# Performance work log

Hardware: AMD Instinct MI355X
Metric: run time of the kernel (lower is better)

Reference implementation:

```python
import jax, jax.numpy as jnp
import numpy as np

B, S, HID = 2, 2048, 2048
H, HKV, D = 16, 8, 128
CHUNK = 512
THETA = 1000000.0
NEG = -1e9


def setup_inputs() -> dict:
    key = jax.random.key(0)
    ks = jax.random.split(key, 10)
    hidden_states = jax.random.normal(ks[0], (B, S, HID), dtype=jnp.float32)
    # additive causal mask (0 on/below diagonal, -1e9 above)
    tri = jnp.tril(jnp.ones((S, S), dtype=bool))
    attention_mask = jnp.where(tri, 0.0, NEG).astype(jnp.float32)
    attention_mask = jnp.broadcast_to(attention_mask[None, None], (B, 1, S, S))
    w = 0.02
    Wq = jax.random.normal(ks[1], (HID, H * D), dtype=jnp.float32) * w
    bq = jax.random.normal(ks[2], (H * D,), dtype=jnp.float32) * w
    Wk = jax.random.normal(ks[3], (HID, HKV * D), dtype=jnp.float32) * w
    bk = jax.random.normal(ks[4], (HKV * D,), dtype=jnp.float32) * w
    Wv = jax.random.normal(ks[5], (HID, HKV * D), dtype=jnp.float32) * w
    bv = jax.random.normal(ks[6], (HKV * D,), dtype=jnp.float32) * w
    Wo = jax.random.normal(ks[7], (H * D, HID), dtype=jnp.float32) * w
    bo = jax.random.normal(ks[8], (HID,), dtype=jnp.float32) * w
    return {"hidden_states": hidden_states, "attention_mask": attention_mask,
            "Wq": Wq, "bq": bq, "Wk": Wk, "bk": bk, "Wv": Wv, "bv": bv,
            "Wo": Wo, "bo": bo}


def _rope_tables(seq_len, dim):
    inv_freq = 1.0 / (THETA ** (jnp.arange(0, dim, 2, dtype=jnp.float32) / dim))
    pos = jnp.arange(seq_len, dtype=jnp.float32)
    freqs = pos[:, None] * inv_freq[None, :]          # [S, D/2]
    emb = jnp.concatenate([freqs, freqs], axis=-1)    # [S, D]
    return jnp.cos(emb)[None, None], jnp.sin(emb)[None, None]  # [1,1,S,D]


def _rotate_half(x):
    x1, x2 = jnp.split(x, 2, axis=-1)
    return jnp.concatenate([-x2, x1], axis=-1)


def _attn_forward(hidden_states, attention_mask, Wq, bq, Wk, bk, Wv, bv, Wo, bo):
    bsz, s, _ = hidden_states.shape
    q = (hidden_states @ Wq + bq).reshape(bsz, s, H, D).transpose(0, 2, 1, 3)
    k = (hidden_states @ Wk + bk).reshape(bsz, s, HKV, D).transpose(0, 2, 1, 3)
    v = (hidden_states @ Wv + bv).reshape(bsz, s, HKV, D).transpose(0, 2, 1, 3)
    cos, sin = _rope_tables(s, D)
    q = q * cos + _rotate_half(q) * sin
    k = k * cos + _rotate_half(k) * sin
    n_rep = H // HKV
    k = jnp.repeat(k, n_rep, axis=1)  # repeat_kv
    v = jnp.repeat(v, n_rep, axis=1)
    scale = 1.0 / jnp.sqrt(jnp.float32(D))
    nq, nk = s // CHUNK, s // CHUNK
    Qc = q.reshape(bsz, H, nq, CHUNK, D)
    Kc = jnp.moveaxis(k.reshape(bsz, H, nk, CHUNK, D), 2, 0)   # [nk,B,H,Ck,D]
    Vc = jnp.moveaxis(v.reshape(bsz, H, nk, CHUNK, D), 2, 0)
    Mc = jnp.moveaxis(attention_mask.reshape(bsz, 1, nq, CHUNK, nk, CHUNK), 4, 0)  # [nk,B,1,nq,Cq,Ck]

    def step(carry, xs):
        o, m, d = carry
        k_seg, v_seg, m_seg = xs
        # scores: [B,H,nq,Cq,Ck]
        sc = jnp.einsum('bhqcd,bhkd->bhqck', Qc, k_seg) * scale + m_seg
        new_m = jnp.maximum(m, sc.max(axis=-1, keepdims=True))
        e = jnp.exp(sc - new_m)
        sums = e.sum(axis=-1, keepdims=True)
        prev = jnp.exp(m - new_m)          # NOTE: uses running max, as in source
        d_new = prev + sums
        o = (o * prev + jnp.einsum('bhqck,bhkd->bhqcd', e, v_seg)) / d_new
        return (o, new_m, d_new), None

    o0 = jnp.zeros((bsz, H, nq, CHUNK, D), dtype=jnp.float32)
    m0 = jnp.full((bsz, H, nq, CHUNK, 1), -jnp.inf, dtype=jnp.float32)
    d0 = jnp.ones((bsz, H, nq, CHUNK, 1), dtype=jnp.float32)
    (o, m, d), _ = jax.lax.scan(step, (o0, m0, d0), (Kc, Vc, Mc))
    # final rescale: attn_output * exp(max - logsumexp) == o / d_last (source math)
    o = o / d
    attn = o.reshape(bsz, H, s, D).transpose(0, 2, 1, 3).reshape(bsz, s, H * D)
    return attn @ Wo + bo


def reference(hidden_states, attention_mask, Wq, bq, Wk, bk, Wv, bv, Wo, bo):
    return _attn_forward(hidden_states, attention_mask, Wq, bq, Wk, bk, Wv, bv, Wo, bo)
```

## Files before the change

kernel.cpp:

```cpp
#include <hip/hip_runtime.h>
#include <hip/hip_bf16.h>


typedef __attribute__((ext_vector_type(8))) short s8v;
typedef __attribute__((ext_vector_type(4))) float f4v;
typedef __attribute__((ext_vector_type(4))) unsigned int u32x4;

#define MFMA16(a, b, c) __builtin_amdgcn_mfma_f32_16x16x32_bf16((a), (b), (c), 0, 0, 0)

typedef unsigned short u16;
typedef const __attribute__((address_space(1))) unsigned int* gas_p;
typedef __attribute__((address_space(3))) unsigned int* las_p;

template <bool B> struct BoolC { static constexpr bool value = B; };

__device__ __forceinline__ void gl_lds16(const void* g, void* l) {
    __builtin_amdgcn_global_load_lds((gas_p)g, (las_p)l, 16, 0, 0);
}

__device__ __forceinline__ u16 f2b(float f) {
    __hip_bfloat16 h = __float2bfloat16(f);
    return *reinterpret_cast<u16*>(&h);
}
__device__ __forceinline__ float b2f(u16 u) {
    __hip_bfloat16 h;
    *reinterpret_cast<u16*>(&h) = u;
    return __bfloat162float(h);
}

__device__ __forceinline__ void qswap(unsigned int& a, unsigned int& b) {
#if __has_builtin(__builtin_amdgcn_permlane32_swap) && __has_builtin(__builtin_amdgcn_permlane16_swap)
    typedef __attribute__((ext_vector_type(2))) unsigned int u32x2;
    u32x2 r1 = __builtin_amdgcn_permlane32_swap(a, b, false, false);
    u32x2 r2 = __builtin_amdgcn_permlane16_swap(r1[0], r1[1], false, false);
    a = r2[0]; b = r2[1];
#else
    asm volatile("v_permlane32_swap_b32 %0, %1\n\t"
                 "s_nop 0\n\t"
                 "v_permlane16_swap_b32 %0, %1\n\t"
                 "s_nop 0"
                 : "+v"(a), "+v"(b));
#endif
}

__device__ const unsigned char qt_tab[40] = {
    4, 5, 6, 7,
    8, 8, 9, 9, 10, 10, 11, 11,
    12, 12, 12, 13, 13, 13, 14, 14, 14, 15, 15, 15,
    3, 7, 11, 15, 2, 6, 10, 14, 1, 5, 9, 13, 0, 4, 8, 12};
__device__ const unsigned char c_tab[40] = {
    0, 0, 0, 0,
    0, 1, 0, 1, 0, 1, 0, 1,
    0, 1, 2, 0, 1, 2, 0, 1, 2, 0, 1, 2,
    0, 1, 2, 3, 0, 1, 2, 3, 0, 1, 2, 3, 0, 1, 2, 3};

__device__ __forceinline__ int uoff40(int qt, int c) {
    int qc = qt >> 2;
    if (c < qc) {
        if (qt < 8) return qt - 4;
        if (qt < 12) return 4 + ((qt - 8) << 1) + c;
        return 12 + (qt - 12) * 3 + c;
    }
    return 24 + ((3 - (qt & 3)) << 2) + qc;
}

__global__ __launch_bounds__(256) void k_cast_hs(const float* __restrict__ src,
                                                 u16* __restrict__ dst) {
    int i = blockIdx.x * 256 + threadIdx.x;
    float4 v = reinterpret_cast<const float4*>(src)[i];
    alignas(8) u16 t[4] = {f2b(v.x), f2b(v.y), f2b(v.z), f2b(v.w)};
    reinterpret_cast<uint2*>(dst)[i] = *reinterpret_cast<uint2*>(t);
}

__global__ __launch_bounds__(256) void k_transpose_w(
    const float* __restrict__ Wq, const float* __restrict__ Wk,
    const float* __restrict__ Wv, const float* __restrict__ Wo,
    u16* __restrict__ wt_all, u16* __restrict__ wo_t) {
    int id = blockIdx.x;
    const float* W; u16* dst; int N, nbase;
    if (id < 4096)      { W = Wq; dst = wt_all; N = 2048; nbase = 0; }
    else if (id < 6144) { W = Wk; dst = wt_all; N = 1024; nbase = 2048; id -= 4096; }
    else if (id < 8192) { W = Wv; dst = wt_all; N = 1024; nbase = 3072; id -= 6144; }
    else                { W = Wo; dst = wo_t;  N = 2048; nbase = 0;    id -= 8192; }
    int tiles_n = N >> 5;
    int k0 = (id / tiles_n) << 5, n0 = (id % tiles_n) << 5;
    __shared__ float t[32][33];
    int tid = threadIdx.x;
    {
        int row = tid >> 3, c4 = (tid & 7) << 2;
        float4 v = *reinterpret_cast<const float4*>(&W[(size_t)(k0 + row) * N + n0 + c4]);
        t[row][c4 + 0] = v.x; t[row][c4 + 1] = v.y;
        t[row][c4 + 2] = v.z; t[row][c4 + 3] = v.w;
    }
    __syncthreads();
    {
        int n = tid >> 3, kq = (tid & 7) << 2;
        alignas(8) u16 p[4];
#pragma unroll
        for (int j = 0; j < 4; j++) p[j] = f2b(t[kq + j][n]);
        *reinterpret_cast<uint2*>(&dst[(size_t)(nbase + n0 + n) * 2048 + k0 + kq]) =
            *reinterpret_cast<uint2*>(p);
    }
}

__global__ __launch_bounds__(256) void k_bias(const float* __restrict__ bq,
                                              const float* __restrict__ bk,
                                              const float* __restrict__ bv,
                                              float* __restrict__ dst) {
    int i = blockIdx.x * 256 + threadIdx.x;
    float v = (i < 2048) ? bq[i] : (i < 3072) ? bk[i - 2048] : bv[i - 3072];
    dst[i] = v;
}

__global__ __launch_bounds__(256) void k_gemm(
    const u16* __restrict__ A, const u16* __restrict__ Bt,
    const float* __restrict__ bias, void* __restrict__ out,
    int M, int N, int K, int out_f32) {
    __shared__ alignas(16) u16 As[2][128][64];
    __shared__ alignas(16) u16 Bs[2][128][64];
    int tid = threadIdx.x;
    int wave = tid >> 6, lane = tid & 63, quad = lane >> 4, l16 = lane & 15;
    int nwg = gridDim.x * gridDim.y;
    int wg = blockIdx.y * gridDim.x + blockIdx.x;
    int l = (wg & 7) * (nwg >> 3) + (wg >> 3);
    int t4 = l >> 4, a4 = l & 15;
    int tn4 = gridDim.x >> 2;
    int tm = t4 / tn4, tn = t4 % tn4;
    int m0 = ((tm << 2) + (a4 >> 2)) << 7;
    int n0 = ((tn << 2) + (a4 & 3)) << 7;
    int wm = (wave >> 1) << 6, wn = (wave & 1) << 6;
    f4v zero = {0.f, 0.f, 0.f, 0.f};
    f4v acc[4][4];
#pragma unroll
    for (int a = 0; a < 4; a++)
#pragma unroll
        for (int b = 0; b < 4; b++) acc[a][b] = zero;
    int r0 = tid >> 3;
    int gsw = (tid & 7) ^ (r0 & 7);
    const u16* gA = A + (size_t)(m0 + r0) * K + (gsw << 3);
    const u16* gB = Bt + (size_t)(n0 + r0) * K + (gsw << 3);
    auto stage = [&](int k0, int buf) {
#pragma unroll
        for (int i = 0; i < 4; i++) {
            gl_lds16(gA + (size_t)(i << 5) * K + k0,
                     (char*)&As[buf][0][0] + (i << 12) + tid * 16);
            gl_lds16(gB + (size_t)(i << 5) * K + k0,
                     (char*)&Bs[buf][0][0] + (i << 12) + tid * 16);
        }
    };
    int NT = K >> 6;
    stage(0, 0);
    __syncthreads();
    for (int t = 0; t < NT; t++) {
        int cur = t & 1;
        if (t + 1 < NT) stage((t + 1) << 6, cur ^ 1);
#pragma unroll
        for (int ks = 0; ks < 2; ks++) {
            int rg = (((ks << 2) | quad) ^ (l16 & 7)) << 3;
            s8v af[4], bf_[4];
#pragma unroll
            for (int mi = 0; mi < 4; mi++)
                af[mi] = *reinterpret_cast<const s8v*>(&As[cur][wm + mi * 16 + l16][rg]);
#pragma unroll
            for (int ni = 0; ni < 4; ni++)
                bf_[ni] = *reinterpret_cast<const s8v*>(&Bs[cur][wn + ni * 16 + l16][rg]);
#pragma unroll
            for (int mi = 0; mi < 4; mi++)
#pragma unroll
                for (int ni = 0; ni < 4; ni++)
                    acc[mi][ni] = MFMA16(af[mi], bf_[ni], acc[mi][ni]);
        }
        __syncthreads();
    }
    if (!out_f32) {
        u16* cs = &As[0][0][0];
#pragma unroll
        for (int ni = 0; ni < 4; ni++) {
            float bsv = bias[n0 + wn + ni * 16 + l16];
#pragma unroll
            for (int mi = 0; mi < 4; mi++)
#pragma unroll
                for (int r = 0; r < 4; r++)
                    cs[(wm + mi * 16 + (quad << 2) + r) * 128 + wn + ni * 16 + l16] =
                        f2b(acc[mi][ni][r] + bsv);
        }
        __syncthreads();
        int row = tid >> 1, c0 = (tid & 1) << 6;
        u16* dst = (u16*)out + (size_t)(m0 + row) * N + n0 + c0;
#pragma unroll
        for (int j = 0; j < 8; j++)
            *reinterpret_cast<uint4*>(dst + j * 8) =
                *reinterpret_cast<const uint4*>(&cs[row * 128 + c0 + j * 8]);
    } else {
        float* cf = (float*)&As[0][0][0];
#pragma unroll
        for (int p = 0; p < 2; p++) {
            __syncthreads();
            if ((wm >> 6) == p) {
#pragma unroll
                for (int ni = 0; ni < 4; ni++) {
                    float bsv = bias[n0 + wn + ni * 16 + l16];
#pragma unroll
                    for (int mi = 0; mi < 4; mi++)
#pragma unroll
                        for (int r = 0; r < 4; r++)
                            cf[((wm - (p << 6)) + mi * 16 + (quad << 2) + r) * 128 +
                               wn + ni * 16 + l16] = acc[mi][ni][r] + bsv;
                }
            }
            __syncthreads();
            int row = tid >> 2, q4 = (tid & 3) << 5;
            float* dst = (float*)out + (size_t)(m0 + (p << 6) + row) * N + n0 + q4;
#pragma unroll
            for (int j = 0; j < 8; j++)
                *reinterpret_cast<uint4*>(dst + j * 4) =
                    *reinterpret_cast<const uint4*>(&cf[row * 128 + q4 + j * 4]);
        }
    }
}

__global__ __launch_bounds__(256) void k_rope(const u16* __restrict__ qkv,
                                              u16* __restrict__ qr,
                                              u16* __restrict__ kr) {
    const float qscale = 0.08838834764831845f * 1.44269504088896340f;
    int row = blockIdx.x;
    int b = row >> 11, s = row & 2047;
    const u16* src = qkv + (size_t)row * 4096;
    __shared__ float lcs[64], lsn[64];
    int tid = threadIdx.x;
    if (tid < 64) {
        float fr = (float)s * exp2f((float)tid * -0.31143075889569023f);
        lcs[tid] = cosf(fr);
        lsn[tid] = sinf(fr);
    }
    __syncthreads();
    for (int u = tid; u < 1536; u += 256) {
        int hh, i;
        const u16* sp;
        u16* dp;
        float sc;
        if (u < 1024) {
            hh = u >> 6; i = u & 63;
            sp = src + hh * 128;
            dp = qr + ((size_t)(b * 16 + hh) * 2048 + s) * 128;
            sc = qscale;
        } else {
            int u2 = u - 1024;
            hh = u2 >> 6; i = u2 & 63;
            sp = src + 2048 + hh * 128;
            dp = kr + ((size_t)(b * 8 + hh) * 2048 + s) * 128;
            sc = 1.f;
        }
        float x1 = b2f(sp[i]);
        float x2 = b2f(sp[i + 64]);
        float cs = lcs[i], sn = lsn[i];
        dp[i]      = f2b((x1 * cs - x2 * sn) * sc);
        dp[i + 64] = f2b((x2 * cs + x1 * sn) * sc);
    }
}

__global__ __launch_bounds__(256) void k_vtrans(const u16* __restrict__ qkv,
                                                u16* __restrict__ vt) {
    int bkv = blockIdx.z, b = bkv >> 3, kv = bkv & 7;
    int s0 = blockIdx.x << 6, d0 = blockIdx.y << 5;
    __shared__ alignas(16) u16 t[32][72];
    int tid = threadIdx.x, c = tid & 31, rr = tid >> 5;
#pragma unroll
    for (int i = 0; i < 8; i++) {
        int s = s0 + rr + i * 8;
        t[c][rr + i * 8] = qkv[(size_t)(b * 2048 + s) * 4096 + 3072 + kv * 128 + d0 + c];
    }
    __syncthreads();
    int dd = tid >> 3, sc8 = (tid & 7) << 3;
    *reinterpret_cast<uint4*>(&vt[((size_t)(b * 8 + kv) * 128 + d0 + dd) * 2048 + s0 + sc8]) =
        *reinterpret_cast<const uint4*>(&t[dd][sc8]);
}

__global__ __launch_bounds__(256, 3) void k_attn_part(const u16* __restrict__ qr,
                                                      const u16* __restrict__ kr,
                                                      const u16* __restrict__ vt,
                                                      u16* __restrict__ PVp,
                                                      float* __restrict__ scp) {
    const float NINF = -__builtin_inff();
    __shared__ alignas(16) u16 Ks[2][64 * 128];
    __shared__ alignas(16) u16 Vs[128 * 64];

    int tid = threadIdx.x;
    int wv = tid >> 6, lane = tid & 63, quad = lane >> 4, l16 = lane & 15;
    int x = blockIdx.x, h = blockIdx.y, b = blockIdx.z, kvh = h >> 1;
    int qt = qt_tab[x], c = c_tab[x], qc = qt >> 2;
    bool diag = (c == qc);
    int m3 = qt & 3;
    int nt = diag ? ((m3 + 1) << 1) : 8;
    int kbase = c << 9;
    const u16* Qp = qr + ((size_t)(b * 16 + h) * 2048 + qt * 128 + wv * 32) * 128;
    const u16* Kp = kr + ((size_t)(b * 8 + kvh) * 2048) * 128;
    const u16* Vp = vt + ((size_t)(b * 8 + kvh) * 128) * 2048;

    s8v qf0[4], qf1[4];
#pragma unroll
    for (int sl = 0; sl < 4; sl++) {
        qf0[sl] = *reinterpret_cast<const s8v*>(&Qp[l16 * 128 + sl * 32 + (quad << 3)]);
        qf1[sl] = *reinterpret_cast<const s8v*>(&Qp[(16 + l16) * 128 + sl * 32 + (quad << 3)]);
    }
    s8v ones;
#pragma unroll
    for (int i = 0; i < 8; i++) ones[i] = (short)0x3F80;
    s8v pzero;
#pragma unroll
    for (int i = 0; i < 8; i++) pzero[i] = (short)0;

    int krow = tid >> 4, kg = (tid & 15) ^ krow;
    int vd = tid >> 3, vg = (tid & 7) ^ (vd & 7);
    auto stageK = [&](int t) {
        int kbt = kbase + (t << 6);
        const u16* kgp = Kp + (size_t)(kbt + krow) * 128 + (kg << 3);
        char* kd = (char*)&Ks[t & 1][0];
#pragma unroll
        for (int i = 0; i < 4; i++)
            gl_lds16(kgp + (size_t)(i << 4) * 128, kd + (i << 12) + tid * 16);
    };
    auto stageV = [&](int t) {
        int kbt = kbase + (t << 6);
        const u16* vgp = Vp + (size_t)vd * 2048 + kbt + (vg << 3);
        char* vdst = (char*)&Vs[0];
#pragma unroll
        for (int i = 0; i < 4; i++)
            gl_lds16(vgp + (size_t)(i << 5) * 2048, vdst + (i << 12) + tid * 16);
    };

    auto pack = [&](const f4v& s, bool tri, bool act, float& tmx,
                    unsigned int& wlo, unsigned int& whi) {
        if (!act) { wlo = 0u; whi = 0u; return; }
        float e[4];
#pragma unroll
        for (int r = 0; r < 4; r++) {
            float v = s[r];
            if (tri && ((quad << 2) + r > l16)) v = NINF;
            tmx = fmaxf(tmx, v);
            e[r] = __builtin_amdgcn_exp2f(v);
        }
        wlo = (unsigned int)f2b(e[0]) | ((unsigned int)f2b(e[1]) << 16);
        whi = (unsigned int)f2b(e[2]) | ((unsigned int)f2b(e[3]) << 16);
    };

    f4v zero = {0.f, 0.f, 0.f, 0.f};
    f4v u0[8], u1[8], sums0 = zero, sums1 = zero;
#pragma unroll
    for (int ni = 0; ni < 8; ni++) { u0[ni] = zero; u1[ni] = zero; }
    float tmx0 = NINF, tmx1 = NINF;
    int qg0 = wv << 1, qg1 = (wv << 1) + 1;

    auto run = [&](auto diagc) {
        constexpr bool DIAG = decltype(diagc)::value;
        stageK(0);
        for (int t = 0; t < nt; t++) {
            __syncthreads();
            stageV(t);
            if (t + 1 < nt) stageK(t + 1);
            const char* Kbuf = (const char*)&Ks[t & 1][0];
            int kgb = DIAG ? ((t << 2) - (m3 << 3)) : 0;
            s8v pa0s[2], pa1s[2];
            bool act0[2], act1[2];
#pragma unroll
            for (int s2 = 0; s2 < 2; s2++) {
                int kgA = kgb + (s2 << 1), kgB = kgA + 1;
                bool skip = DIAG && (kgA > qg1);
                bool a0 = !DIAG || (kgA <= qg0);
                bool b0 = !DIAG || (kgB <= qg0);
                bool b1 = !DIAG || (kgB <= qg1);
                act1[s2] = !skip;
                act0[s2] = !skip && a0;
                if (skip) { pa0s[s2] = pzero; pa1s[s2] = pzero; continue; }
                f4v sA0 = zero, sA1 = zero, sB0 = zero, sB1 = zero;
#pragma unroll
                for (int sl = 0; sl < 4; sl++) {
                    s8v kf = *reinterpret_cast<const s8v*>(
                        Kbuf + (((s2 << 1) << 4) + l16) * 256 +
                        ((((sl << 2) + quad) ^ l16) << 4));
                    if (a0) sA0 = MFMA16(kf, qf0[sl], sA0);
                    sA1 = MFMA16(kf, qf1[sl], sA1);
                }
                if (b1) {
#pragma unroll
                    for (int sl = 0; sl < 4; sl++) {
                        s8v kf = *reinterpret_cast<const s8v*>(
                            Kbuf + ((((s2 << 1) | 1) << 4) + l16) * 256 +
                            ((((sl << 2) + quad) ^ l16) << 4));
                        if (b0) sB0 = MFMA16(kf, qf0[sl], sB0);
                        sB1 = MFMA16(kf, qf1[sl], sB1);
                    }
                }
                unsigned int A0w, A1w, B0w, B1w;
                pack(sA1, DIAG && (kgA == qg1), true, tmx1, A0w, A1w);
                pack(sB1, DIAG && (kgB == qg1), b1, tmx1, B0w, B1w);
                qswap(A0w, B0w); qswap(A1w, B1w);
                u32x4 pw1 = {A0w, A1w, B0w, B1w};
                pa1s[s2] = __builtin_bit_cast(s8v, pw1);
                if (a0) {
                    unsigned int C0w, C1w, D0w, D1w;
                    pack(sA0, DIAG && (kgA == qg0), true, tmx0, C0w, C1w);
                    pack(sB0, DIAG && (kgB == qg0), b0, tmx0, D0w, D1w);
                    qswap(C0w, D0w); qswap(C1w, D1w);
                    u32x4 pw0 = {C0w, C1w, D0w, D1w};
                    pa0s[s2] = __builtin_bit_cast(s8v, pw0);
                } else {
                    pa0s[s2] = pa1s[s2];
                }
            }
            __syncthreads();
#pragma unroll
            for (int s2 = 0; s2 < 2; s2++) {
                if (DIAG && !act1[s2]) continue;
                bool a0 = !DIAG || act0[s2];
                if (a0) sums0 = MFMA16(pa0s[s2], ones, sums0);
                sums1 = MFMA16(pa1s[s2], ones, sums1);
#pragma unroll
                for (int ni = 0; ni < 8; ni++) {
                    s8v vf = *reinterpret_cast<const s8v*>(
                        (const char*)&Vs[0] + ((ni << 4) + l16) * 128 +
                        ((((s2 << 2) + quad) ^ (l16 & 7)) << 4));
                    if (a0) u0[ni] = MFMA16(pa0s[s2], vf, u0[ni]);
                    u1[ni] = MFMA16(pa1s[s2], vf, u1[ni]);
                }
            }
        }
    };
    if (diag) run(BoolC<true>{}); else run(BoolC<false>{});

    tmx0 = fmaxf(tmx0, __shfl_xor(tmx0, 16));
    tmx0 = fmaxf(tmx0, __shfl_xor(tmx0, 32));
    tmx1 = fmaxf(tmx1, __shfl_xor(tmx1, 16));
    tmx1 = fmaxf(tmx1, __shfl_xor(tmx1, 32));
    float m0[4], m1[4], resc0[4], resc1[4];
#pragma unroll
    for (int r = 0; r < 4; r++) {
        m0[r] = __shfl(tmx0, (quad << 2) + r);
        m1[r] = __shfl(tmx1, (quad << 2) + r);
        resc0[r] = __builtin_amdgcn_exp2f(-m0[r]);
        resc1[r] = __builtin_amdgcn_exp2f(-m1[r]);
    }
    int slot = (b * 16 + h) * 40 + x;
    u16* pvdst = PVp + (size_t)slot * 16384;
    int row0 = wv * 32 + (quad << 2);
#pragma unroll
    for (int ni = 0; ni < 8; ni++)
#pragma unroll
        for (int r = 0; r < 4; r++) {
            pvdst[(row0 + r) * 128 + ni * 16 + l16] = f2b(u0[ni][r] * resc0[r]);
            pvdst[(row0 + 16 + r) * 128 + ni * 16 + l16] = f2b(u1[ni][r] * resc1[r]);
        }
    if (l16 == 0) {
        float* scd = scp + (size_t)slot * 256 + row0;
#pragma unroll
        for (int r = 0; r < 4; r++) {
            scd[r] = m0[r] * 0.6931471805599453f;
            scd[16 + r] = m1[r] * 0.6931471805599453f;
            scd[128 + r] = sums0[r] * resc0[r];
            scd[144 + r] = sums1[r] * resc1[r];
        }
    }
}

__global__ __launch_bounds__(256) void k_attn_comb(const u16* __restrict__ PVp,
                                                   const float* __restrict__ scp,
                                                   u16* __restrict__ attnb) {
    int qt64 = blockIdx.x, h = blockIdx.y, b = blockIdx.z;
    int qt = qt64 >> 1, qc = qt >> 2;
    int tid = threadIdx.x;
    int row = ((qt64 & 1) << 6) + (tid >> 2), d0 = (tid & 3) << 5;
    int bh = b * 16 + h;
    float o[32];
#pragma unroll
    for (int i = 0; i < 32; i++) o[i] = 0.f;
    float mprev = -__builtin_inff(), dlast = 1.f;
    for (int cc = 0; cc <= qc; cc++) {
        int slot = bh * 40 + uoff40(qt, cc);
        float ch = scp[(size_t)slot * 256 + row];
        float sh = scp[(size_t)slot * 256 + 128 + row];
        float mnew = fmaxf(mprev, ch);
        float p = __expf(mprev - mnew);
        float lam = __expf(ch - mnew);
        float dd = p + lam * sh;
        float inv = 1.f / dd;
        const u16* pv = PVp + (size_t)slot * 16384 + row * 128 + d0;
#pragma unroll
        for (int k = 0; k < 4; k++) {
            s8v v8 = *reinterpret_cast<const s8v*>(pv + (k << 3));
#pragma unroll
            for (int j = 0; j < 8; j++) {
                int i = (k << 3) + j;
                o[i] = (o[i] * p + lam * b2f((u16)v8[j])) * inv;
            }
        }
        mprev = mnew;
        dlast = dd;
    }
    if (qc == 3) {
        float inv = 1.f / dlast;
#pragma unroll
        for (int i = 0; i < 32; i++) o[i] *= inv;
    }
    alignas(16) u16 ob[32];
#pragma unroll
    for (int i = 0; i < 32; i++) ob[i] = f2b(o[i]);
    u16* dst = attnb + (size_t)(b * 2048 + qt * 128 + row) * 2048 + h * 128 + d0;
#pragma unroll
    for (int k = 0; k < 4; k++)
        reinterpret_cast<uint4*>(dst)[k] = reinterpret_cast<const uint4*>(ob)[k];
}

extern "C" void kernel_launch(void* const* d_in, const int* in_sizes, int n_in,
                              void* d_out, int out_size, void* d_ws, size_t ws_size,
                              hipStream_t stream) {
    (void)in_sizes; (void)n_in; (void)out_size; (void)ws_size;
    const float* hs = (const float*)d_in[0];
    const float* Wq = (const float*)d_in[2];
    const float* bq = (const float*)d_in[3];
    const float* Wk = (const float*)d_in[4];
    const float* bk = (const float*)d_in[5];
    const float* Wv = (const float*)d_in[6];
    const float* bv = (const float*)d_in[7];
    const float* Wo = (const float*)d_in[8];
    const float* bo = (const float*)d_in[9];

    char* ws = (char*)d_ws;
    u16* hsb      = (u16*)(ws);
    u16* qr       = hsb;
    u16* attnb    = hsb;
    u16* wt_all   = (u16*)(ws + (16u << 20));
    u16* kr       = wt_all;
    u16* vt       = (u16*)(ws + (24u << 20));
    u16* wo_t     = (u16*)(ws + (32u << 20));
    float* bias_c = (float*)(ws + (40u << 20));
    u16* qkv      = (u16*)(ws + (40u << 20) + 65536);
    u16* PVp      = qkv;
    float* scp    = (float*)(ws + (40u << 20) + 65536 + 41943040u);

    k_cast_hs<<<8192, 256, 0, stream>>>(hs, hsb);
    k_transpose_w<<<12288, 256, 0, stream>>>(Wq, Wk, Wv, Wo, wt_all, wo_t);
    k_bias<<<16, 256, 0, stream>>>(bq, bk, bv, bias_c);
    k_gemm<<<dim3(32, 32), 256, 0, stream>>>(hsb, wt_all, bias_c, qkv,
                                             4096, 4096, 2048, 0);
    k_rope<<<4096, 256, 0, stream>>>(qkv, qr, kr);
    k_vtrans<<<dim3(32, 4, 16), 256, 0, stream>>>(qkv, vt);
    k_attn_part<<<dim3(40, 16, 2), 256, 0, stream>>>(qr, kr, vt, PVp, scp);
    k_attn_comb<<<dim3(32, 16, 2), 256, 0, stream>>>(PVp, scp, attnb);
    k_gemm<<<dim3(16, 32), 256, 0, stream>>>(attnb, wo_t, bo, d_out,
                                             4096, 2048, 2048, 1);
}
```

Before: 364.8 us.

## Prefetch GEMM tiles two ahead with explicit vmcnt waits; swizzle epilogue LDS

Restructures the GEMM main loop so two K-tiles are in flight. It waits with s_waitcnt vmcnt(8) for only the current tile, then issues the load for tile t+2 into the just-freed buffer after a raw barrier. The aim is to hide global-to-LDS latency better than the previous single-stage prefetch with full __syncthreads. It also XOR-swizzles the LDS staging layout in both the bf16 and fp32 epilogues to reduce bank conflicts on the transposed write-out. The hand-written waitcnts rely on each stage issuing exactly 8 loads, so the code is fragile if that count changes.

```diff
diff --git a/kernel.cpp b/kernel.cpp
--- a/kernel.cpp
+++ b/kernel.cpp
@@ -150,10 +150,16 @@
     };
     int NT = K >> 6;
     stage(0, 0);
-    __syncthreads();
+    stage(64, 1);
     for (int t = 0; t < NT; t++) {
         int cur = t & 1;
-        if (t + 1 < NT) stage((t + 1) << 6, cur ^ 1);
+        if (t + 1 < NT)
+            asm volatile("s_waitcnt vmcnt(8)" ::: "memory");
+        else
+            asm volatile("s_waitcnt vmcnt(0)" ::: "memory");
+        __builtin_amdgcn_sched_barrier(0);
+        __builtin_amdgcn_s_barrier();
+        __builtin_amdgcn_sched_barrier(0);
 #pragma unroll
         for (int ks = 0; ks < 2; ks++) {
             int rg = (((ks << 2) | quad) ^ (l16 & 7)) << 3;
@@ -170,27 +176,36 @@
                 for (int ni = 0; ni < 4; ni++)
                     acc[mi][ni] = MFMA16(af[mi], bf_[ni], acc[mi][ni]);
         }
-        __syncthreads();
+        asm volatile("s_waitcnt lgkmcnt(0)" ::: "memory");
+        __builtin_amdgcn_sched_barrier(0);
+        __builtin_amdgcn_s_barrier();
+        __builtin_amdgcn_sched_barrier(0);
+        if (t + 2 < NT) stage((t + 2) << 6, cur);
     }
     if (!out_f32) {
         u16* cs = &As[0][0][0];
 #pragma unroll
         for (int ni = 0; ni < 4; ni++) {
-            float bsv = bias[n0 + wn + ni * 16 + l16];
+            int col = wn + ni * 16 + l16;
+            float bsv = bias[n0 + col];
 #pragma unroll
             for (int mi = 0; mi < 4; mi++)
 #pragma unroll
-                for (int r = 0; r < 4; r++)
-                    cs[(wm + mi * 16 + (quad << 2) + r) * 128 + wn + ni * 16 + l16] =
+                for (int r = 0; r < 4; r++) {
+                    int row = wm + mi * 16 + (quad << 2) + r;
+                    cs[row * 128 + ((((col >> 3) ^ (row & 7)) << 3) | (col & 7))] =
                         f2b(acc[mi][ni][r] + bsv);
+                }
         }
         __syncthreads();
-        int row = tid >> 1, c0 = (tid & 1) << 6;
-        u16* dst = (u16*)out + (size_t)(m0 + row) * N + n0 + c0;
-#pragma unroll
-        for (int j = 0; j < 8; j++)
+        int row = tid >> 1, c8 = (tid & 1) << 3;
+        u16* dst = (u16*)out + (size_t)(m0 + row) * N + n0 + (c8 << 3);
+#pragma unroll
+        for (int j = 0; j < 8; j++) {
+            int g = (c8 + j) ^ (row & 7);
             *reinterpret_cast<uint4*>(dst + j * 8) =
-                *reinterpret_cast<const uint4*>(&cs[row * 128 + c0 + j * 8]);
+                *reinterpret_cast<const uint4*>(&cs[row * 128 + g * 8]);
+        }
     } else {
         float* cf = (float*)&As[0][0][0];
 #pragma unroll
@@ -199,22 +214,27 @@
             if ((wm >> 6) == p) {
 #pragma unroll
                 for (int ni = 0; ni < 4; ni++) {
-                    float bsv = bias[n0 + wn + ni * 16 + l16];
+                    int col = wn + ni * 16 + l16;
+                    float bsv = bias[n0 + col];
 #pragma unroll
                     for (int mi = 0; mi < 4; mi++)
 #pragma unroll
-                        for (int r = 0; r < 4; r++)
-                            cf[((wm - (p << 6)) + mi * 16 + (quad << 2) + r) * 128 +
-                               wn + ni * 16 + l16] = acc[mi][ni][r] + bsv;
+                        for (int r = 0; r < 4; r++) {
+                            int lr = (wm - (p << 6)) + mi * 16 + (quad << 2) + r;
+                            cf[lr * 128 + ((((col >> 2) ^ (lr & 7)) << 2) | (col & 3))] =
+                                acc[mi][ni][r] + bsv;
+                        }
                 }
             }
             __syncthreads();
-            int row = tid >> 2, q4 = (tid & 3) << 5;
-            float* dst = (float*)out + (size_t)(m0 + (p << 6) + row) * N + n0 + q4;
-#pragma unroll
-            for (int j = 0; j < 8; j++)
+            int row = tid >> 2, g0 = (tid & 3) << 3;
+            float* dst = (float*)out + (size_t)(m0 + (p << 6) + row) * N + n0 + (g0 << 2);
+#pragma unroll
+            for (int j = 0; j < 8; j++) {
+                int g = (g0 + j) ^ (row & 7);
                 *reinterpret_cast<uint4*>(dst + j * 4) =
-                    *reinterpret_cast<const uint4*>(&cf[row * 128 + q4 + j * 4]);
+                    *reinterpret_cast<const uint4*>(&cf[row * 128 + g * 4]);
+            }
         }
     }
 }
```

Result: slower. 377.7 us (+3.6%).
